# Performance work log

Hardware: AMD Instinct MI355X
Metric: run time of the kernel (lower is better)

The kernel has to match this reference:

```python
import jax, jax.numpy as jnp
import numpy as np

B, N, DIM, H, DH = 4, 2048, 1024, 16, 64

def setup_inputs() -> dict:
    key = jax.random.key(0)
    k1, k2, k3 = jax.random.split(key, 3)
    x = jax.random.normal(k1, (B, N, DIM), dtype=jnp.float32)
    mask = jnp.ones((B, N), dtype=bool)
    w_qkv = jax.random.normal(k2, (DIM, 3 * H * DH), dtype=jnp.float32) * (DIM ** -0.5)
    w_out = jax.random.normal(k3, (H * DH, DIM), dtype=jnp.float32) * ((H * DH) ** -0.5)
    b_out = jnp.zeros((DIM,), dtype=jnp.float32)
    return {"x": x, "mask": mask, "w_qkv": w_qkv, "w_out": w_out, "b_out": b_out}

def reference(x, mask, w_qkv, w_out, b_out):
    b, n, _ = x.shape
    h, dh = H, DH
    scale = dh ** -0.5
    qkv = x @ w_qkv  # [b, n, 3*h*dh]
    q, k, v = jnp.split(qkv, 3, axis=-1)
    # [b, n, h*dh] -> [b, h, n, dh]
    reshape = lambda t: t.reshape(b, n, h, dh).transpose(0, 2, 1, 3)
    q, k, v = reshape(q) * scale, reshape(k), reshape(v)
    dots = jnp.einsum('bhid,bhjd->bhij', q, k)  # materialized N x N scores
    neg = -jnp.finfo(dots.dtype).max
    # key padding mask: [b, j] -> [b, 1, 1, j]
    dots = jnp.where(mask[:, None, None, :], dots, neg)
    # causal mask: mask out j > i
    causal = jnp.triu(jnp.ones((n, n), dtype=bool), k=1)
    dots = jnp.where(causal[None, None, :, :], neg, dots)
    attn = jax.nn.softmax(dots, axis=-1)
    out = jnp.einsum('bhij,bhjd->bhid', attn, v)
    out = out.transpose(0, 2, 1, 3).reshape(b, n, h * dh)
    return out @ w_out + b_out
```

## Files before the change

### kernel.cpp

```cpp
#include <hip/hip_runtime.h>

#define B_   4
#define N_   2048
#define DIM_ 1024
#define H_   16
#define DH_  64
#define NT   (B_ * N_)
#define PS   ((size_t)B_ * H_ * N_ * DH_)

typedef __bf16 bf16x8 __attribute__((ext_vector_type(8)));
typedef short  s16x4  __attribute__((ext_vector_type(4)));
typedef float  f32x4  __attribute__((ext_vector_type(4)));
typedef unsigned int   u32;
typedef unsigned int   u32x2 __attribute__((ext_vector_type(2)));
typedef unsigned short u16;

#define LOG2E 1.44269504088896f
#define QSCALE (0.125f * LOG2E)

__device__ __forceinline__ u16 f2bf(float f) {
  u32 u = __float_as_uint(f);
  u += 0x7FFFu + ((u >> 16) & 1u);
  return (u16)(u >> 16);
}

__device__ __forceinline__ u32 bfpack(float f0, float f1) {
  u32 a = __float_as_uint(f0) + 0x8000u;
  u32 b = __float_as_uint(f1) + 0x8000u;
  return __builtin_amdgcn_perm(b, a, 0x07060302);
}

__device__ __forceinline__ float fexp2(float x) {
  return __builtin_amdgcn_exp2f(x);
}

__device__ __forceinline__ f32x4 mfma32(bf16x8 a, bf16x8 b, f32x4 c) {
  return __builtin_amdgcn_mfma_f32_16x16x32_bf16(a, b, c, 0, 0, 0);
}
__device__ __forceinline__ f32x4 mfma16k(s16x4 a, s16x4 b, f32x4 c) {
  return __builtin_amdgcn_mfma_f32_16x16x16bf16_1k(a, b, c, 0, 0, 0);
}

__device__ __forceinline__ void gld16(const void* g, void* l) {
  __builtin_amdgcn_global_load_lds(
      (const __attribute__((address_space(1))) u32*)g,
      (__attribute__((address_space(3))) u32*)l, 16, 0, 0);
}

__device__ __forceinline__ void transpose_body(
    const float* __restrict__ w, u16* __restrict__ wt,
    int K, int Ncols, int bx, int by, int tid, u16* T ) {
  const int n0 = bx * 64, k0 = by * 64;
  const int r = tid >> 4, c4 = (tid & 15) * 4;
#pragma unroll
  for (int i = 0; i < 4; ++i) {
    int row = r + i * 16;
    float4 f = *(const float4*)(w + (size_t)(k0 + row) * Ncols + n0 + c4);
    u16* p = &T[row * 66 + c4];
    p[0] = f2bf(f.x); p[1] = f2bf(f.y); p[2] = f2bf(f.z); p[3] = f2bf(f.w);
  }
  __syncthreads();
  const int nr = tid >> 2, kc = (tid & 3) * 16;
  u32 p[8];
#pragma unroll
  for (int j = 0; j < 8; ++j)
    p[j] = (u32)T[(kc + 2 * j) * 66 + nr] | ((u32)T[(kc + 2 * j + 1) * 66 + nr] << 16);
  size_t dst = (size_t)(n0 + nr) * K + k0 + kc;
  *(uint4*)(wt + dst)     = make_uint4(p[0], p[1], p[2], p[3]);
  *(uint4*)(wt + dst + 8) = make_uint4(p[4], p[5], p[6], p[7]);
}

__global__ __launch_bounds__(256) void prologue_kernel(
    const float* __restrict__ x, u16* __restrict__ xb,
    const float* __restrict__ w_qkv, u16* __restrict__ wqkvT,
    const float* __restrict__ w_out, u16* __restrict__ woutT) {
  __shared__ u16 T[64 * 66];
  const int b = blockIdx.x, tid = threadIdx.x;
  if (b < 4096) {
    size_t i = ((size_t)b * 256 + tid) * 8;
    float4 f0 = *(const float4*)(x + i);
    float4 f1 = *(const float4*)(x + i + 4);
    uint4 o;
    o.x = (u32)f2bf(f0.x) | ((u32)f2bf(f0.y) << 16);
    o.y = (u32)f2bf(f0.z) | ((u32)f2bf(f0.w) << 16);
    o.z = (u32)f2bf(f1.x) | ((u32)f2bf(f1.y) << 16);
    o.w = (u32)f2bf(f1.z) | ((u32)f2bf(f1.w) << 16);
    *(uint4*)(xb + i) = o;
  } else if (b < 4864) {
    int idx = b - 4096;
    transpose_body(w_qkv, wqkvT, 1024, 3072, idx % 48, idx / 48, tid, T);
  } else {
    int idx = b - 4864;
    transpose_body(w_out, woutT, 1024, 1024, idx % 16, idx / 16, tid, T);
  }
}

__global__ __launch_bounds__(256) void qkv_gemm_kernel(
    const u16* __restrict__ xb, const u16* __restrict__ wt,
    u16* __restrict__ q, u16* __restrict__ k, u16* __restrict__ vt) {
  __shared__ alignas(16) u16 As[128 * 64];
  __shared__ alignas(16) u16 Bs[128 * 64];
  const int tid = threadIdx.x, wave = tid >> 6, lane = tid & 63;
  const int quad = lane >> 4, l15 = lane & 15;
  const int wm = (wave >> 1) * 64, wn = (wave & 1) * 64;
  const int m0 = blockIdx.y * 128, n0 = blockIdx.x * 128;
  const int srow = lane >> 3;
  const int schunk = (lane & 7) ^ srow;

  f32x4 acc[4][4] = {};

  for (int kt = 0; kt < DIM_; kt += 64) {
    __syncthreads();
#pragma unroll
    for (int i = 0; i < 4; ++i) {
      int c = wave * 4 + i;
      int row = c * 8 + srow;
      gld16(xb + (size_t)(m0 + row) * DIM_ + kt + schunk * 8, As + c * 512);
      gld16(wt + (size_t)(n0 + row) * DIM_ + kt + schunk * 8, Bs + c * 512);
    }
    __syncthreads();
#pragma unroll
    for (int h = 0; h < 2; ++h) {
      bf16x8 af[4], bfr[4];
#pragma unroll
      for (int mi = 0; mi < 4; ++mi) {
        int row = wm + mi * 16 + l15;
        af[mi] = *(const bf16x8*)(As + row * 64 + (((quad + 4 * h) ^ (row & 7)) * 8));
      }
#pragma unroll
      for (int ni = 0; ni < 4; ++ni) {
        int row = wn + ni * 16 + l15;
        bfr[ni] = *(const bf16x8*)(Bs + row * 64 + (((quad + 4 * h) ^ (row & 7)) * 8));
      }
#pragma unroll
      for (int ni = 0; ni < 4; ++ni)
#pragma unroll
        for (int mi = 0; mi < 4; ++mi)
          acc[mi][ni] = mfma32(af[mi], bfr[ni], acc[mi][ni]);
    }
  }

#pragma unroll
  for (int ni = 0; ni < 4; ++ni) {
    int colg = n0 + wn + ni * 16 + l15;
    int part = colg >> 10, rem = colg & 1023;
    int hh = rem >> 6, d = rem & 63;
#pragma unroll
    for (int mi = 0; mi < 4; ++mi) {
      int row0 = m0 + wm + mi * 16 + quad * 4;
      int bb = row0 >> 11, nn0 = row0 & 2047;
      size_t bh = (size_t)(bb * H_ + hh);
      if (part == 0) {
#pragma unroll
        for (int r = 0; r < 4; ++r)
          q[(bh * N_ + nn0 + r) * DH_ + d] = f2bf(acc[mi][ni][r] * QSCALE);
      } else if (part == 1) {
#pragma unroll
        for (int r = 0; r < 4; ++r)
          k[(bh * N_ + nn0 + r) * DH_ + d] = f2bf(acc[mi][ni][r]);
      } else {
        u32 lo = bfpack(acc[mi][ni][0], acc[mi][ni][1]);
        u32 hi = bfpack(acc[mi][ni][2], acc[mi][ni][3]);
        *(uint2*)(vt + (bh * DH_ + d) * N_ + nn0) = make_uint2(lo, hi);
      }
    }
  }
}

__global__ __launch_bounds__(512, 8) void attn_kernel(
    const u16* __restrict__ q, const u16* __restrict__ k,
    const u16* __restrict__ vt, u16* __restrict__ ctx) {
  __shared__ alignas(16) u16 Ks[2 * 64 * 64];
  __shared__ alignas(16) u16 Vs[2 * 64 * 64];
  const int tid = threadIdx.x, wave = tid >> 6, lane = tid & 63;
  const int quad = lane >> 4, l15 = lane & 15;
  const int head = blockIdx.x;
  const int p = blockIdx.y;
  const int hh = head & 15, bb = head >> 4;
  const int wgrp = wave >> 2, wsub = wave & 3;
  const int qt = wgrp ? (31 - p) : p;

  const size_t bhofs = (size_t)(bb * H_ + hh) << 17;
  const u16* qp = q + bhofs;
  const u16* kp = k + bhofs;
  const u16* vp = vt + bhofs;

  const int row = qt * 64 + wsub * 16 + l15;
  const bf16x8 qf0 = *(const bf16x8*)(qp + (size_t)row * 64 + quad * 8);
  const bf16x8 qf1 = *(const bf16x8*)(qp + (size_t)row * 64 + 32 + quad * 8);

  float l_s = 0.f;
  f32x4 o[4] = {};

  const int srow8 = lane >> 3;
  const int sslot = (lane & 7) ^ srow8;
  const u16* kstage = kp + (size_t)(wave * 8 + srow8) * 64 + sslot * 8;
  const u16* vstage = vp + (size_t)(wave * 8 + srow8) * N_ + sslot * 8;

  const int smax = 31 - p;

  gld16(kstage, Ks + wave * 512);
  gld16(vstage, Vs + wave * 512);

  for (int s = 0; s <= smax; ++s) {
    if (s < smax) {
      int pn = (s + 1) & 1;
      gld16(kstage + (size_t)(s + 1) * 4096, Ks + pn * 4096 + wave * 512);
      gld16(vstage + (size_t)(s + 1) * 64,   Vs + pn * 4096 + wave * 512);
      asm volatile("s_waitcnt vmcnt(2)" ::: "memory");
    } else {
      asm volatile("s_waitcnt vmcnt(0)" ::: "memory");
    }
    __builtin_amdgcn_s_barrier();
    __builtin_amdgcn_sched_barrier(0);

    if (s <= qt) {
      const int h = s & 1;
      const int kbm = (s == qt) ? wsub : 3;
      const bool needmask = (s == qt);
      const int rowrel = row - s * 64;
      const u16* Kh = Ks + h * 4096;
      const u16* Vh = Vs + h * 4096;
#pragma unroll
      for (int kb = 0; kb < 4; ++kb) {
        if (kb <= kbm) {
          int rk = kb * 16 + l15;
          bf16x8 k0 = *(const bf16x8*)(Kh + rk * 64 + ((quad ^ (rk & 7)) * 8));
          bf16x8 k1 = *(const bf16x8*)(Kh + rk * 64 + (((quad + 4) ^ (rk & 7)) * 8));
          f32x4 z = {};
          z = mfma32(k0, qf0, z);
          z = mfma32(k1, qf1, z);
          if (needmask) {
#pragma unroll
            for (int r = 0; r < 4; ++r)
              if (kb * 16 + quad * 4 + r > rowrel) z[r] = -INFINITY;
          }
          float p0 = fexp2(z[0]), p1 = fexp2(z[1]);
          float p2 = fexp2(z[2]), p3 = fexp2(z[3]);
          l_s += (p0 + p1) + (p2 + p3);
          u32x2 pp = {bfpack(p0, p1), bfpack(p2, p3)};
          s16x4 pbv = __builtin_bit_cast(s16x4, pp);
          int f = 2 * kb + (quad >> 1);
#pragma unroll
          for (int db = 0; db < 4; ++db) {
            int rv = db * 16 + l15;
            int ch = f ^ (rv & 7);
            s16x4 vf = *(const s16x4*)(Vh + rv * 64 + ch * 8 + (quad & 1) * 4);
            o[db] = mfma16k(vf, pbv, o[db]);
          }
        }
      }
    }
    __builtin_amdgcn_sched_barrier(0);
    __builtin_amdgcn_s_barrier();
  }

  l_s += __shfl_xor(l_s, 16);
  l_s += __shfl_xor(l_s, 32);

  {
    float inv = 1.0f / l_s;
    int token = bb * N_ + row;
#pragma unroll
    for (int db = 0; db < 4; ++db) {
      u32 lo = bfpack(o[db][0] * inv, o[db][1] * inv);
      u32 hi = bfpack(o[db][2] * inv, o[db][3] * inv);
      *(uint2*)(ctx + (size_t)token * DIM_ + hh * DH_ + db * 16 + quad * 4) =
          make_uint2(lo, hi);
    }
  }
}

__global__ __launch_bounds__(256) void out_gemm_kernel(
    const u16* __restrict__ cb, const u16* __restrict__ wt,
    const float* __restrict__ bias, float* __restrict__ out) {
  __shared__ alignas(16) u16 As[128 * 64];
  __shared__ alignas(16) u16 Bs[128 * 64];
  const int tid = threadIdx.x, wave = tid >> 6, lane = tid & 63;
  const int quad = lane >> 4, l15 = lane & 15;
  const int wm = (wave >> 1) * 64, wn = (wave & 1) * 64;
  const int m0 = blockIdx.y * 128, n0 = blockIdx.x * 128;
  const int srow = lane >> 3;
  const int schunk = (lane & 7) ^ srow;

  f32x4 acc[4][4] = {};

  for (int kt = 0; kt < DIM_; kt += 64) {
    __syncthreads();
#pragma unroll
    for (int i = 0; i < 4; ++i) {
      int c = wave * 4 + i;
      int row = c * 8 + srow;
      gld16(cb + (size_t)(m0 + row) * DIM_ + kt + schunk * 8, As + c * 512);
      gld16(wt + (size_t)(n0 + row) * DIM_ + kt + schunk * 8, Bs + c * 512);
    }
    __syncthreads();
#pragma unroll
    for (int h = 0; h < 2; ++h) {
      bf16x8 af[4], bfr[4];
#pragma unroll
      for (int mi = 0; mi < 4; ++mi) {
        int row = wm + mi * 16 + l15;
        af[mi] = *(const bf16x8*)(As + row * 64 + (((quad + 4 * h) ^ (row & 7)) * 8));
      }
#pragma unroll
      for (int ni = 0; ni < 4; ++ni) {
        int row = wn + ni * 16 + l15;
        bfr[ni] = *(const bf16x8*)(Bs + row * 64 + (((quad + 4 * h) ^ (row & 7)) * 8));
      }
#pragma unroll
      for (int ni = 0; ni < 4; ++ni)
#pragma unroll
        for (int mi = 0; mi < 4; ++mi)
          acc[mi][ni] = mfma32(af[mi], bfr[ni], acc[mi][ni]);
    }
  }

#pragma unroll
  for (int ni = 0; ni < 4; ++ni) {
    int col = n0 + wn + ni * 16 + l15;
    float bv = bias[col];
#pragma unroll
    for (int mi = 0; mi < 4; ++mi) {
      int row0 = m0 + wm + mi * 16 + quad * 4;
#pragma unroll
      for (int r = 0; r < 4; ++r)
        out[(size_t)(row0 + r) * DIM_ + col] = acc[mi][ni][r] + bv;
    }
  }
}

extern "C" void kernel_launch(void* const* d_in, const int* in_sizes, int n_in,
                              void* d_out, int out_size, void* d_ws, size_t ws_size,
                              hipStream_t stream) {
  (void)in_sizes; (void)n_in; (void)out_size; (void)ws_size;
  const float* x     = (const float*)d_in[0];
  const float* w_qkv = (const float*)d_in[2];
  const float* w_out = (const float*)d_in[3];
  const float* b_out = (const float*)d_in[4];
  float* out = (float*)d_out;

  u16* xb_ctx = (u16*)d_ws;
  u16* qw     = xb_ctx + (size_t)NT * DIM_;
  u16* kw     = qw + PS;
  u16* vw     = kw + PS;
  u16* wqkvT  = vw + PS;
  u16* woutT  = wqkvT + (size_t)3072 * 1024;

  prologue_kernel<<<5120, 256, 0, stream>>>(x, xb_ctx, w_qkv, wqkvT, w_out, woutT);
  qkv_gemm_kernel<<<dim3(24, 64), 256, 0, stream>>>(xb_ctx, wqkvT, qw, kw, vw);
  attn_kernel<<<dim3(64, 16), 512, 0, stream>>>(qw, kw, vw, xb_ctx);
  out_gemm_kernel<<<dim3(8, 64), 256, 0, stream>>>(xb_ctx, woutT, b_out, out);
}
```

Measured before the change: 240.1 us.

## Double-buffer LDS tiles in QKV and output GEMMs with async prefetch

Both projection GEMMs now keep two LDS stages for the A and B tiles. The next K-tile is issued with direct-to-LDS loads while the MFMA work on the current tile runs, and explicit vmcnt waits plus barriers order the two stages. This is meant to hide global-load latency behind compute, where before every iteration serialised load and compute. In exchange, shared memory per block doubles, which may lower occupancy.

```diff
diff --git a/kernel.cpp b/kernel.cpp
--- a/kernel.cpp
+++ b/kernel.cpp
@@ -98,8 +98,8 @@
 __global__ __launch_bounds__(256) void qkv_gemm_kernel(
     const u16* __restrict__ xb, const u16* __restrict__ wt,
     u16* __restrict__ q, u16* __restrict__ k, u16* __restrict__ vt) {
-  __shared__ alignas(16) u16 As[128 * 64];
-  __shared__ alignas(16) u16 Bs[128 * 64];
+  __shared__ alignas(16) u16 As[2 * 128 * 64];
+  __shared__ alignas(16) u16 Bs[2 * 128 * 64];
   const int tid = threadIdx.x, wave = tid >> 6, lane = tid & 63;
   const int quad = lane >> 4, l15 = lane & 15;
   const int wm = (wave >> 1) * 64, wn = (wave & 1) * 64;
@@ -107,30 +107,48 @@
   const int srow = lane >> 3;
   const int schunk = (lane & 7) ^ srow;
 
+  const u16* asrc = xb + (size_t)(m0 + srow) * DIM_ + schunk * 8;
+  const u16* bsrc = wt + (size_t)(n0 + srow) * DIM_ + schunk * 8;
+
   f32x4 acc[4][4] = {};
 
-  for (int kt = 0; kt < DIM_; kt += 64) {
-    __syncthreads();
-#pragma unroll
-    for (int i = 0; i < 4; ++i) {
-      int c = wave * 4 + i;
-      int row = c * 8 + srow;
-      gld16(xb + (size_t)(m0 + row) * DIM_ + kt + schunk * 8, As + c * 512);
-      gld16(wt + (size_t)(n0 + row) * DIM_ + kt + schunk * 8, Bs + c * 512);
-    }
-    __syncthreads();
+#pragma unroll
+  for (int i = 0; i < 4; ++i) {
+    int c = wave * 4 + i;
+    gld16(asrc + (size_t)(c * 8) * DIM_, As + c * 512);
+    gld16(bsrc + (size_t)(c * 8) * DIM_, Bs + c * 512);
+  }
+
+  for (int t = 0; t < 16; ++t) {
+    if (t < 15) {
+      int pn = (t + 1) & 1;
+#pragma unroll
+      for (int i = 0; i < 4; ++i) {
+        int c = wave * 4 + i;
+        gld16(asrc + (size_t)(c * 8) * DIM_ + (t + 1) * 64, As + pn * 8192 + c * 512);
+        gld16(bsrc + (size_t)(c * 8) * DIM_ + (t + 1) * 64, Bs + pn * 8192 + c * 512);
+      }
+      asm volatile("s_waitcnt vmcnt(8)" ::: "memory");
+    } else {
+      asm volatile("s_waitcnt vmcnt(0)" ::: "memory");
+    }
+    __builtin_amdgcn_s_barrier();
+    __builtin_amdgcn_sched_barrier(0);
+
+    const u16* Ab = As + (t & 1) * 8192;
+    const u16* Bb = Bs + (t & 1) * 8192;
 #pragma unroll
     for (int h = 0; h < 2; ++h) {
       bf16x8 af[4], bfr[4];
 #pragma unroll
       for (int mi = 0; mi < 4; ++mi) {
         int row = wm + mi * 16 + l15;
-        af[mi] = *(const bf16x8*)(As + row * 64 + (((quad + 4 * h) ^ (row & 7)) * 8));
+        af[mi] = *(const bf16x8*)(Ab + row * 64 + (((quad + 4 * h) ^ (row & 7)) * 8));
       }
 #pragma unroll
       for (int ni = 0; ni < 4; ++ni) {
         int row = wn + ni * 16 + l15;
-        bfr[ni] = *(const bf16x8*)(Bs + row * 64 + (((quad + 4 * h) ^ (row & 7)) * 8));
+        bfr[ni] = *(const bf16x8*)(Bb + row * 64 + (((quad + 4 * h) ^ (row & 7)) * 8));
       }
 #pragma unroll
       for (int ni = 0; ni < 4; ++ni)
@@ -138,6 +156,8 @@
         for (int mi = 0; mi < 4; ++mi)
           acc[mi][ni] = mfma32(af[mi], bfr[ni], acc[mi][ni]);
     }
+    __builtin_amdgcn_sched_barrier(0);
+    __builtin_amdgcn_s_barrier();
   }
 
 #pragma unroll
@@ -274,8 +294,8 @@
 __global__ __launch_bounds__(256) void out_gemm_kernel(
     const u16* __restrict__ cb, const u16* __restrict__ wt,
     const float* __restrict__ bias, float* __restrict__ out) {
-  __shared__ alignas(16) u16 As[128 * 64];
-  __shared__ alignas(16) u16 Bs[128 * 64];
+  __shared__ alignas(16) u16 As[2 * 128 * 64];
+  __shared__ alignas(16) u16 Bs[2 * 128 * 64];
   const int tid = threadIdx.x, wave = tid >> 6, lane = tid & 63;
   const int quad = lane >> 4, l15 = lane & 15;
   const int wm = (wave >> 1) * 64, wn = (wave & 1) * 64;
@@ -283,30 +303,48 @@
   const int srow = lane >> 3;
   const int schunk = (lane & 7) ^ srow;
 
+  const u16* asrc = cb + (size_t)(m0 + srow) * DIM_ + schunk * 8;
+  const u16* bsrc = wt + (size_t)(n0 + srow) * DIM_ + schunk * 8;
+
   f32x4 acc[4][4] = {};
 
-  for (int kt = 0; kt < DIM_; kt += 64) {
-    __syncthreads();
-#pragma unroll
-    for (int i = 0; i < 4; ++i) {
-      int c = wave * 4 + i;
-      int row = c * 8 + srow;
-      gld16(cb + (size_t)(m0 + row) * DIM_ + kt + schunk * 8, As + c * 512);
-      gld16(wt + (size_t)(n0 + row) * DIM_ + kt + schunk * 8, Bs + c * 512);
-    }
-    __syncthreads();
+#pragma unroll
+  for (int i = 0; i < 4; ++i) {
+    int c = wave * 4 + i;
+    gld16(asrc + (size_t)(c * 8) * DIM_, As + c * 512);
+    gld16(bsrc + (size_t)(c * 8) * DIM_, Bs + c * 512);
+  }
+
+  for (int t = 0; t < 16; ++t) {
+    if (t < 15) {
+      int pn = (t + 1) & 1;
+#pragma unroll
+      for (int i = 0; i < 4; ++i) {
+        int c = wave * 4 + i;
+        gld16(asrc + (size_t)(c * 8) * DIM_ + (t + 1) * 64, As + pn * 8192 + c * 512);
+        gld16(bsrc + (size_t)(c * 8) * DIM_ + (t + 1) * 64, Bs + pn * 8192 + c * 512);
+      }
+      asm volatile("s_waitcnt vmcnt(8)" ::: "memory");
+    } else {
+      asm volatile("s_waitcnt vmcnt(0)" ::: "memory");
+    }
+    __builtin_amdgcn_s_barrier();
+    __builtin_amdgcn_sched_barrier(0);
+
+    const u16* Ab = As + (t & 1) * 8192;
+    const u16* Bb = Bs + (t & 1) * 8192;
 #pragma unroll
     for (int h = 0; h < 2; ++h) {
       bf16x8 af[4], bfr[4];
 #pragma unroll
       for (int mi = 0; mi < 4; ++mi) {
         int row = wm + mi * 16 + l15;
-        af[mi] = *(const bf16x8*)(As + row * 64 + (((quad + 4 * h) ^ (row & 7)) * 8));
+        af[mi] = *(const bf16x8*)(Ab + row * 64 + (((quad + 4 * h) ^ (row & 7)) * 8));
       }
 #pragma unroll
       for (int ni = 0; ni < 4; ++ni) {
         int row = wn + ni * 16 + l15;
-        bfr[ni] = *(const bf16x8*)(Bs + row * 64 + (((quad + 4 * h) ^ (row & 7)) * 8));
+        bfr[ni] = *(const bf16x8*)(Bb + row * 64 + (((quad + 4 * h) ^ (row & 7)) * 8));
       }
 #pragma unroll
       for (int ni = 0; ni < 4; ++ni)
@@ -314,6 +352,8 @@
         for (int mi = 0; mi < 4; ++mi)
           acc[mi][ni] = mfma32(af[mi], bfr[ni], acc[mi][ni]);
     }
+    __builtin_amdgcn_sched_barrier(0);
+    __builtin_amdgcn_s_barrier();
   }
 
 #pragma unroll
```

New measurement: 244.5 us (median of 4 runs). Within noise of the previous version (+1.8%).
